# Optimization experiments

Hardware: AMD Instinct MI355X
Metric: run time of the kernel (lower is better)

The kernel has to match this reference:

```python
import jax, jax.numpy as jnp
import numpy as np

N_NODES = 100000
N_EDGES = 1600000
IN_DIM = 128
OUT_DIM = 128


def setup_inputs() -> dict:
    key = jax.random.key(0)
    k1, k2, k3, k4, k5 = jax.random.split(key, 5)
    x = jax.random.normal(k1, (N_NODES, IN_DIM), dtype=jnp.float32)
    edge_src = jax.random.randint(k2, (N_EDGES,), 0, N_NODES, dtype=jnp.int32)
    edge_dst = jax.random.randint(k3, (N_EDGES,), 0, N_NODES, dtype=jnp.int32)
    # nn.Linear(in_dim*2, out_dim): W stored here as [2*in_dim, out_dim] (already transposed)
    W = jax.random.normal(k4, (2 * IN_DIM, OUT_DIM), dtype=jnp.float32) * (1.0 / np.sqrt(2 * IN_DIM))
    b = jax.random.normal(k5, (OUT_DIM,), dtype=jnp.float32) * 0.01
    return {"x": x, "edge_src": edge_src, "edge_dst": edge_dst, "W": W, "b": b}


def reference(x, edge_src, edge_dst, W, b):
    # adj_mean @ x  ==  mean over neighbors: sum_j x[src_j] into row dst_j, / deg(dst)
    n = x.shape[0]
    deg = jax.ops.segment_sum(jnp.ones_like(edge_dst, dtype=x.dtype), edge_dst, num_segments=n)
    deg = jnp.maximum(deg, 1.0)  # rows with no neighbors -> zero vector (0/1)
    neigh = jax.ops.segment_sum(x[edge_src], edge_dst, num_segments=n) / deg[:, None]
    # concat([x, neigh], dim=1) then Linear
    out = jnp.concatenate([x, neigh], axis=1) @ W + b
    return out
```

## Files before the change

kernel.cpp:

```cpp
#include <hip/hip_runtime.h>

#define IN_DIM 128
#define OUT_DIM 128
#define PADCAP 1792
#define EPB 8192

typedef short bf16x8 __attribute__((ext_vector_type(8)));
typedef float f32x4 __attribute__((ext_vector_type(4)));
typedef float f32x2 __attribute__((ext_vector_type(2)));
typedef unsigned int u32x4 __attribute__((ext_vector_type(4)));

__device__ __forceinline__ unsigned short f2bf(float f) {
    union { float f; unsigned int u; } v; v.f = f;
    unsigned int u = v.u;
    u += 0x7FFFu + ((u >> 16) & 1u);
    return (unsigned short)(u >> 16);
}

__global__ __launch_bounds__(256) void prep_kernel(const float* __restrict__ x,
                                                   unsigned char* __restrict__ xq,
                                                   const float* __restrict__ W,
                                                   unsigned short* __restrict__ WF,
                                                   int* __restrict__ cursor,
                                                   int nN, int total8, int nconv, int nb) {
    const int b = blockIdx.x;
    const int t = threadIdx.x;
    if (b < nconv) {
        int i = b * 256 + t;
        if (i >= total8) return;
        const float4* p = (const float4*)x + (size_t)i * 2;
        float4 v0 = p[0], v1 = p[1];
        int w0 = 0, w1 = 0;
        w0 = __builtin_amdgcn_cvt_pk_fp8_f32(v0.x, v0.y, w0, false);
        w0 = __builtin_amdgcn_cvt_pk_fp8_f32(v0.z, v0.w, w0, true);
        w1 = __builtin_amdgcn_cvt_pk_fp8_f32(v1.x, v1.y, w1, false);
        w1 = __builtin_amdgcn_cvt_pk_fp8_f32(v1.z, v1.w, w1, true);
        uint2 o; o.x = (unsigned int)w0; o.y = (unsigned int)w1;
        int node = i >> 4, oct = i & 15;
        int q = oct >> 2, o8 = oct & 3;
        *(uint2*)(xq + (size_t)q * (nN + 1) * 32 + (size_t)node * 32 + o8 * 8) = o;
    } else if (b < nconv + 16) {
        int tt = (b - nconv) * 256 + t;
        int frag = tt >> 6, lane = tt & 63;
        int f = frag >> 3, c = frag & 7;
        int col = c * 16 + (lane & 15);
        int kbase = f * 32 + (lane >> 4) * 8;
        bf16x8 h;
#pragma unroll
        for (int i = 0; i < 8; i++)
            h[i] = (short)f2bf(W[(size_t)(kbase + i) * OUT_DIM + col]);
        *(bf16x8*)(WF + (size_t)tt * 8) = h;
    } else if (b == nconv + 16) {
        if (t < 32) {
            int q = t >> 3, o = t & 7;
            *(unsigned int*)(xq + (size_t)q * (nN + 1) * 32 + (size_t)nN * 32 + o * 4) = 0u;
        }
    } else {
        int i = (b - nconv - 17) * 256 + t;
        if (i < nb) cursor[i] = i * PADCAP;
    }
}

__global__ __launch_bounds__(1024) void place_kernel(const int* __restrict__ src,
                                                     const int* __restrict__ dst,
                                                     int* __restrict__ cursor,
                                                     unsigned int* __restrict__ csr_packed,
                                                     int nE, int nb) {
    __shared__ int lcnt[2048];
    __shared__ int lbase[2048];
    const int t = threadIdx.x;
    for (int i = t; i < nb; i += 1024) lcnt[i] = 0;
    __syncthreads();
    const int e0 = blockIdx.x * EPB;
    unsigned int meta[EPB / 1024];
#pragma unroll
    for (int k = 0; k < EPB / 1024; k++) {
        int e = e0 + k * 1024 + t;
        if (e < nE) {
            int d = dst[e];
            int bk = d >> 6, dl = d & 63;
            int r = atomicAdd(&lcnt[bk], 1);
            meta[k] = ((unsigned)bk << 20) | ((unsigned)dl << 14) | (unsigned)r;
        } else meta[k] = 0xFFFFFFFFu;
    }
    __syncthreads();
    for (int i = t; i < nb; i += 1024) {
        int c = lcnt[i];
        lbase[i] = c ? atomicAdd(&cursor[i], c) : 0;
    }
    __syncthreads();
#pragma unroll
    for (int k = 0; k < EPB / 1024; k++) {
        if (meta[k] != 0xFFFFFFFFu) {
            int e = e0 + k * 1024 + t;
            unsigned int m = meta[k];
            int bk = m >> 20, dl = (m >> 14) & 63, r = m & 0x3FFF;
            csr_packed[lbase[bk] + r] = ((unsigned)dl << 17) | (unsigned)src[e];
        }
    }
}

__global__ __launch_bounds__(256, 8) void qgather_kernel(const unsigned char* __restrict__ xq,
                                                         const unsigned int* __restrict__ csr_packed,
                                                         const int* __restrict__ cursor,
                                                         unsigned short* __restrict__ neigh,
                                                         int nN, int nb) {
    __shared__ unsigned int el[PADCAP];
    __shared__ int bcnt[64];
    __shared__ int bpst[64];
    __shared__ int bst[64];
    __shared__ int bdg[64];
    __shared__ int brw[64];

    const int bid = blockIdx.x;
    const int xcd = bid & 7;
    const int quarter = xcd & 3;
    const int bucket = (bid >> 3) * 2 + (xcd >> 2);
    if (bucket >= nb) return;

    const int t = threadIdx.x;
    const int lane = t & 63;
    const int wave = t >> 6;

    const size_t e0 = (size_t)bucket * PADCAP;
    int n = cursor[bucket] - bucket * PADCAP;
    if (n > PADCAP) n = PADCAP;

    const unsigned int sentinel = (unsigned)nN << 5;
    if (t < 64) bcnt[t] = 0;
#pragma unroll
    for (int k = 0; k < 7; k++) el[k * 256 + t] = sentinel;
    __syncthreads();

    unsigned int pk[7]; int rk[7];
#pragma unroll
    for (int k = 0; k < 7; k++) {
        int idx = k * 256 + t;
        if (idx < n) {
            unsigned int p = csr_packed[e0 + idx];
            pk[k] = p;
            rk[k] = atomicAdd(&bcnt[(p >> 17) & 63], 1);
        } else pk[k] = 0xFFFFFFFFu;
    }
    __syncthreads();

    if (wave == 0) {
        int dg = bcnt[lane];
        int pl = (dg + 7) & ~7;
        int s = pl;
#pragma unroll
        for (int off = 1; off < 64; off <<= 1) {
            int u = __shfl_up(s, off);
            if (lane >= off) s += u;
        }
        bpst[lane] = s - pl;
        unsigned key = ((unsigned)dg << 6) | (unsigned)lane;
#pragma unroll
        for (int k = 2; k <= 64; k <<= 1) {
#pragma unroll
            for (int j = k >> 1; j > 0; j >>= 1) {
                unsigned other = __shfl_xor(key, j);
                bool lower = (lane & j) == 0;
                bool asc   = (lane & k) == 0;
                unsigned mn = min(key, other), mx = max(key, other);
                key = (lower == asc) ? mn : mx;
            }
        }
        int rowid = key & 63;
        bst[lane] = bpst[rowid];
        bdg[lane] = (int)(key >> 6);
        brw[lane] = rowid;
    }
    __syncthreads();

#pragma unroll
    for (int k = 0; k < 7; k++) {
        if (pk[k] != 0xFFFFFFFFu) {
            int dl = (pk[k] >> 17) & 63;
            el[bpst[dl] + rk[k]] = (pk[k] & 0x1FFFFu) << 5;
        }
    }
    __syncthreads();

    const int g = lane >> 2;
    const int c = lane & 3;
    const unsigned char* plane = xq + (size_t)quarter * (nN + 1) * 32 + c * 8;
    const int qoff = quarter * 32;

    const int r  = wave * 16 + g;
    const int st = bst[r];
    const int dg = bdg[r];
    const int pl = (dg + 7) & ~7;
    const unsigned int* ep = el + st;

    f32x2 a0{0.f, 0.f}, a1{0.f, 0.f}, a2{0.f, 0.f}, a3{0.f, 0.f};
    for (int j = 0; j < pl; j += 8) {
#pragma unroll
        for (int u = 0; u < 8; u++) {
            unsigned int s = ep[j + ((u + g) & 7)];
            uint2 v = *(const uint2*)(plane + s);
            f32x2 p;
            p = __builtin_amdgcn_cvt_pk_f32_fp8(v.x, false); a0 += p;
            p = __builtin_amdgcn_cvt_pk_f32_fp8(v.x, true);  a1 += p;
            p = __builtin_amdgcn_cvt_pk_f32_fp8(v.y, false); a2 += p;
            p = __builtin_amdgcn_cvt_pk_f32_fp8(v.y, true);  a3 += p;
        }
    }
    const float rd = 1.0f / (float)((dg > 0) ? dg : 1);
    a0 *= rd; a1 *= rd; a2 *= rd; a3 *= rd;
    unsigned int w0, w1, w2, w3;
    asm("v_cvt_pk_bf16_f32 %0, %1, %2" : "=v"(w0) : "v"(a0.x), "v"(a0.y));
    asm("v_cvt_pk_bf16_f32 %0, %1, %2" : "=v"(w1) : "v"(a1.x), "v"(a1.y));
    asm("v_cvt_pk_bf16_f32 %0, %1, %2" : "=v"(w2) : "v"(a2.x), "v"(a2.y));
    asm("v_cvt_pk_bf16_f32 %0, %1, %2" : "=v"(w3) : "v"(a3.x), "v"(a3.y));
    u32x4 o = {w0, w1, w2, w3};
    const int row = bucket * 64 + brw[r];
    *(u32x4*)(neigh + (size_t)row * IN_DIM + qoff + c * 8) = o;
}

__global__ __launch_bounds__(256, 6) void gemm_kernel(const float* __restrict__ x,
                                                      const unsigned short* __restrict__ neigh,
                                                      const unsigned short* __restrict__ WF,
                                                      const float* __restrict__ bias,
                                                      float* __restrict__ out, int nN) {
    const int t = threadIdx.x;
    const int lane = t & 63;
    const int wave = t >> 6;
    const int row0 = blockIdx.x * 64;

    f32x4 acc[8];
#pragma unroll
    for (int c = 0; c < 8; c++) acc[c] = f32x4{0.f, 0.f, 0.f, 0.f};

    const int arow = wave * 16 + (lane & 15);
    const int koff = (lane >> 4) * 8;
    const int rowc = min(row0 + arow, nN - 1);
    const float*          xrow = x     + (size_t)rowc * IN_DIM;
    const unsigned short* nrow = neigh + (size_t)rowc * IN_DIM;

#pragma unroll
    for (int f = 0; f < 8; f++) {
        bf16x8 af;
        if (f < 4) {
            const float* px = xrow + f * 32 + koff;
            float4 v0 = *(const float4*)px;
            float4 v1 = *(const float4*)(px + 4);
            unsigned int r0, r1, r2, r3;
            asm("v_cvt_pk_bf16_f32 %0, %1, %2" : "=v"(r0) : "v"(v0.x), "v"(v0.y));
            asm("v_cvt_pk_bf16_f32 %0, %1, %2" : "=v"(r1) : "v"(v0.z), "v"(v0.w));
            asm("v_cvt_pk_bf16_f32 %0, %1, %2" : "=v"(r2) : "v"(v1.x), "v"(v1.y));
            asm("v_cvt_pk_bf16_f32 %0, %1, %2" : "=v"(r3) : "v"(v1.z), "v"(v1.w));
            union { unsigned int u[4]; bf16x8 v; } cv;
            cv.u[0] = r0; cv.u[1] = r1; cv.u[2] = r2; cv.u[3] = r3;
            af = cv.v;
        } else {
            af = *(const bf16x8*)(nrow + (f - 4) * 32 + koff);
        }
#pragma unroll
        for (int c = 0; c < 8; c++) {
            bf16x8 bf = *(const bf16x8*)(WF + ((size_t)(f * 8 + c) * 64 + lane) * 8);
            acc[c] = __builtin_amdgcn_mfma_f32_16x16x32_bf16(af, bf, acc[c], 0, 0, 0);
        }
    }

    const int orow0 = row0 + wave * 16 + (lane >> 4) * 4;
    const int ocol  = lane & 15;
#pragma unroll
    for (int c = 0; c < 8; c++) {
        const float bv = bias[c * 16 + ocol];
#pragma unroll
        for (int r = 0; r < 4; r++) {
            int row = orow0 + r;
            if (row < nN)
                out[(size_t)row * OUT_DIM + c * 16 + ocol] = acc[c][r] + bv;
        }
    }
}

extern "C" void kernel_launch(void* const* d_in, const int* in_sizes, int n_in,
                              void* d_out, int out_size, void* d_ws, size_t ws_size,
                              hipStream_t stream) {
    const float* x        = (const float*)d_in[0];
    const int*   edge_src = (const int*)d_in[1];
    const int*   edge_dst = (const int*)d_in[2];
    const float* W        = (const float*)d_in[3];
    const float* bias     = (const float*)d_in[4];
    float* out = (float*)d_out;

    const int nN = in_sizes[0] / IN_DIM;
    const int nE = in_sizes[1];
    const int nb = (nN + 63) >> 6;

    int* cursor = (int*)d_ws;
    unsigned int* csr_packed = (unsigned int*)(cursor + 2048);
    unsigned char* xq = (unsigned char*)(csr_packed + (size_t)nb * PADCAP);
    unsigned short* WF = (unsigned short*)(xq + (size_t)4 * (nN + 1) * 32);
    unsigned short* neigh = WF + 128 * 256;

    const int total8 = nN * IN_DIM / 8;
    const int nconv  = (total8 + 255) / 256;
    const int ninit  = (nb + 255) / 256;
    prep_kernel<<<nconv + 17 + ninit, 256, 0, stream>>>(x, xq, W, WF, cursor,
                                                        nN, total8, nconv, nb);

    const int eblk = (nE + EPB - 1) / EPB;
    place_kernel<<<eblk, 1024, 0, stream>>>(edge_src, edge_dst, cursor, csr_packed, nE, nb);

    const int nbp2 = (nb + 1) / 2;
    qgather_kernel<<<nbp2 * 8, 256, 0, stream>>>(xq, csr_packed, cursor, neigh, nN, nb);
    gemm_kernel<<<(nN + 63) / 64, 256, 0, stream>>>(x, neigh, WF, bias, out, nN);
}
```

Measured before the change: 107.6 us.

## Split fp8 feature planes into halves instead of quarters for gather

Re-lays out the fp8 copy of x as two 64-byte column halves per node instead of four 32-byte quarters. Each gather block now handles one half, so every lane loads 16 bytes per neighbor and keeps eight accumulator pairs. The grid mapping is changed so each XCD pair covers a half. This halves the number of blocks that redo the per-bucket edge sort and shared-memory setup, and makes each gather access wider. The cost is that each half-plane is twice as large, which may reduce L2 locality per XCD, and register use rises.

Measured after the change: 104.8 us. 2.7% less time.

```diff
diff --git a/kernel.cpp b/kernel.cpp
--- a/kernel.cpp
+++ b/kernel.cpp
@@ -37,8 +37,8 @@
         w1 = __builtin_amdgcn_cvt_pk_fp8_f32(v1.z, v1.w, w1, true);
         uint2 o; o.x = (unsigned int)w0; o.y = (unsigned int)w1;
         int node = i >> 4, oct = i & 15;
-        int q = oct >> 2, o8 = oct & 3;
-        *(uint2*)(xq + (size_t)q * (nN + 1) * 32 + (size_t)node * 32 + o8 * 8) = o;
+        int h = oct >> 3, o8 = oct & 7;
+        *(uint2*)(xq + (size_t)h * (nN + 1) * 64 + (size_t)node * 64 + o8 * 8) = o;
     } else if (b < nconv + 16) {
         int tt = (b - nconv) * 256 + t;
         int frag = tt >> 6, lane = tt & 63;
@@ -52,8 +52,8 @@
         *(bf16x8*)(WF + (size_t)tt * 8) = h;
     } else if (b == nconv + 16) {
         if (t < 32) {
-            int q = t >> 3, o = t & 7;
-            *(unsigned int*)(xq + (size_t)q * (nN + 1) * 32 + (size_t)nN * 32 + o * 4) = 0u;
+            int h = t >> 4, o = t & 15;
+            *(unsigned int*)(xq + (size_t)h * (nN + 1) * 64 + (size_t)nN * 64 + o * 4) = 0u;
         }
     } else {
         int i = (b - nconv - 17) * 256 + t;
@@ -114,8 +114,8 @@
 
     const int bid = blockIdx.x;
     const int xcd = bid & 7;
-    const int quarter = xcd & 3;
-    const int bucket = (bid >> 3) * 2 + (xcd >> 2);
+    const int half = xcd & 1;
+    const int bucket = (bid >> 3) * 4 + (xcd >> 1);
     if (bucket >= nb) return;
 
     const int t = threadIdx.x;
@@ -126,7 +126,7 @@
     int n = cursor[bucket] - bucket * PADCAP;
     if (n > PADCAP) n = PADCAP;
 
-    const unsigned int sentinel = (unsigned)nN << 5;
+    const unsigned int sentinel = (unsigned)nN << 6;
     if (t < 64) bcnt[t] = 0;
 #pragma unroll
     for (int k = 0; k < 7; k++) el[k * 256 + t] = sentinel;
@@ -177,15 +177,15 @@
     for (int k = 0; k < 7; k++) {
         if (pk[k] != 0xFFFFFFFFu) {
             int dl = (pk[k] >> 17) & 63;
-            el[bpst[dl] + rk[k]] = (pk[k] & 0x1FFFFu) << 5;
+            el[bpst[dl] + rk[k]] = (pk[k] & 0x1FFFFu) << 6;
         }
     }
     __syncthreads();
 
     const int g = lane >> 2;
     const int c = lane & 3;
-    const unsigned char* plane = xq + (size_t)quarter * (nN + 1) * 32 + c * 8;
-    const int qoff = quarter * 32;
+    const unsigned char* plane = xq + (size_t)half * (nN + 1) * 64 + c * 16;
+    const int hoff = half * 64;
 
     const int r  = wave * 16 + g;
     const int st = bst[r];
@@ -193,29 +193,42 @@
     const int pl = (dg + 7) & ~7;
     const unsigned int* ep = el + st;
 
-    f32x2 a0{0.f, 0.f}, a1{0.f, 0.f}, a2{0.f, 0.f}, a3{0.f, 0.f};
+    f32x2 a0{0.f,0.f}, a1{0.f,0.f}, a2{0.f,0.f}, a3{0.f,0.f},
+          a4{0.f,0.f}, a5{0.f,0.f}, a6{0.f,0.f}, a7{0.f,0.f};
     for (int j = 0; j < pl; j += 8) {
 #pragma unroll
         for (int u = 0; u < 8; u++) {
             unsigned int s = ep[j + ((u + g) & 7)];
-            uint2 v = *(const uint2*)(plane + s);
+            uint4 v = *(const uint4*)(plane + s);
             f32x2 p;
             p = __builtin_amdgcn_cvt_pk_f32_fp8(v.x, false); a0 += p;
             p = __builtin_amdgcn_cvt_pk_f32_fp8(v.x, true);  a1 += p;
             p = __builtin_amdgcn_cvt_pk_f32_fp8(v.y, false); a2 += p;
             p = __builtin_amdgcn_cvt_pk_f32_fp8(v.y, true);  a3 += p;
+            p = __builtin_amdgcn_cvt_pk_f32_fp8(v.z, false); a4 += p;
+            p = __builtin_amdgcn_cvt_pk_f32_fp8(v.z, true);  a5 += p;
+            p = __builtin_amdgcn_cvt_pk_f32_fp8(v.w, false); a6 += p;
+            p = __builtin_amdgcn_cvt_pk_f32_fp8(v.w, true);  a7 += p;
         }
     }
     const float rd = 1.0f / (float)((dg > 0) ? dg : 1);
     a0 *= rd; a1 *= rd; a2 *= rd; a3 *= rd;
-    unsigned int w0, w1, w2, w3;
+    a4 *= rd; a5 *= rd; a6 *= rd; a7 *= rd;
+    unsigned int w0, w1, w2, w3, w4, w5, w6, w7;
     asm("v_cvt_pk_bf16_f32 %0, %1, %2" : "=v"(w0) : "v"(a0.x), "v"(a0.y));
     asm("v_cvt_pk_bf16_f32 %0, %1, %2" : "=v"(w1) : "v"(a1.x), "v"(a1.y));
     asm("v_cvt_pk_bf16_f32 %0, %1, %2" : "=v"(w2) : "v"(a2.x), "v"(a2.y));
     asm("v_cvt_pk_bf16_f32 %0, %1, %2" : "=v"(w3) : "v"(a3.x), "v"(a3.y));
-    u32x4 o = {w0, w1, w2, w3};
+    asm("v_cvt_pk_bf16_f32 %0, %1, %2" : "=v"(w4) : "v"(a4.x), "v"(a4.y));
+    asm("v_cvt_pk_bf16_f32 %0, %1, %2" : "=v"(w5) : "v"(a5.x), "v"(a5.y));
+    asm("v_cvt_pk_bf16_f32 %0, %1, %2" : "=v"(w6) : "v"(a6.x), "v"(a6.y));
+    asm("v_cvt_pk_bf16_f32 %0, %1, %2" : "=v"(w7) : "v"(a7.x), "v"(a7.y));
     const int row = bucket * 64 + brw[r];
-    *(u32x4*)(neigh + (size_t)row * IN_DIM + qoff + c * 8) = o;
+    unsigned short* np = neigh + (size_t)row * IN_DIM + hoff + c * 16;
+    u32x4 olo = {w0, w1, w2, w3};
+    u32x4 ohi = {w4, w5, w6, w7};
+    *(u32x4*)np = olo;
+    *(u32x4*)(np + 8) = ohi;
 }
 
 __global__ __launch_bounds__(256, 6) void gemm_kernel(const float* __restrict__ x,
@@ -294,7 +307,7 @@
     int* cursor = (int*)d_ws;
     unsigned int* csr_packed = (unsigned int*)(cursor + 2048);
     unsigned char* xq = (unsigned char*)(csr_packed + (size_t)nb * PADCAP);
-    unsigned short* WF = (unsigned short*)(xq + (size_t)4 * (nN + 1) * 32);
+    unsigned short* WF = (unsigned short*)(xq + (size_t)2 * (nN + 1) * 64);
     unsigned short* neigh = WF + 128 * 256;
 
     const int total8 = nN * IN_DIM / 8;
@@ -306,7 +319,7 @@
     const int eblk = (nE + EPB - 1) / EPB;
     place_kernel<<<eblk, 1024, 0, stream>>>(edge_src, edge_dst, cursor, csr_packed, nE, nb);
 
-    const int nbp2 = (nb + 1) / 2;
-    qgather_kernel<<<nbp2 * 8, 256, 0, stream>>>(xq, csr_packed, cursor, neigh, nN, nb);
+    const int nbp4 = (nb + 3) / 4;
+    qgather_kernel<<<nbp4 * 8, 256, 0, stream>>>(xq, csr_packed, cursor, neigh, nN, nb);
     gemm_kernel<<<(nN + 63) / 64, 256, 0, stream>>>(x, neigh, WF, bias, out, nN);
 }
```
